# Kernel optimization log

Measured on AMD Instinct MI355X. Metric: run time of the kernel, lower is better.

Reference implementation:

```python
import jax, jax.numpy as jnp
import numpy as np
from jax import lax

B = 65536
N_STEPS = 256
WHEELBASE = 2.7
DT = 0.05
MAX_STEER = float(np.deg2rad(30.0))
MAX_SPEED = 100.0
FRICTION_ROAD = 0.1
FRICTION_AIR = 0.01


def setup_inputs() -> dict:
    key = jax.random.key(0)
    k1, k2, k3, k4, k5, k6 = jax.random.split(key, 6)
    return {
        "start_x": jax.random.normal(k1, (B,), dtype=jnp.float32),
        "start_y": jax.random.normal(k2, (B,), dtype=jnp.float32),
        "start_yaw": jax.random.normal(k3, (B,), dtype=jnp.float32),
        "start_speed": jax.random.uniform(k4, (B,), dtype=jnp.float32) * 20.0,
        "accel": jax.random.normal(k5, (B, N_STEPS), dtype=jnp.float32),
        "steering": jax.random.normal(k6, (B, N_STEPS), dtype=jnp.float32),
    }


def reference(start_x, start_y, start_yaw, start_speed, accel, steering):
    # One scan step = one iteration of the original python loop, vectorized over B.
    def step(carry, ctrl):
        x, y, yaw, sp = carry
        a, st = ctrl
        friction = sp * FRICTION_ROAD + FRICTION_AIR * sp * sp
        sp_next = jnp.clip(sp + DT * (a - friction), 0.0, MAX_SPEED)
        steer = jnp.clip(st, -MAX_STEER, MAX_STEER)
        ang_vel = sp * jnp.tan(steer) / WHEELBASE
        x_next = x + sp * jnp.cos(yaw) * DT
        y_next = y + sp * jnp.sin(yaw) * DT
        yaw_next = yaw + ang_vel * DT
        new = (x_next, y_next, yaw_next, sp_next)
        return new, new

    # Controls for steps 0..n_steps-2 (last control unused, as in the original loop).
    ctrls = (accel[:, : N_STEPS - 1].T, steering[:, : N_STEPS - 1].T)  # [T-1, B]
    init = (start_x, start_y, start_yaw, start_speed)
    _, traj = lax.scan(step, init, ctrls)  # each leaf [T-1, B]

    def full(s0, rest):
        return jnp.concatenate([s0[None, :], rest], axis=0).T  # [B, T]

    x = full(start_x, traj[0])
    y = full(start_y, traj[1])
    yaw = full(start_yaw, traj[2])
    speed = full(start_speed, traj[3])
    return (x, y, yaw, speed)
```

## Files before the change

### kernel.cpp

```cpp
#include <hip/hip_runtime.h>

#define T 256
#define TC 16
#define SC 32
#define NSC (T / SC)
#define V 64
#define DT 0.05f
#define WHEELBASE 2.7f
#define MAX_STEER 0.5235987755982988f
#define MAX_SPEED 100.0f
#define FR 0.1f
#define FA 0.01f

__device__ __forceinline__ void lds_fence() {
    asm volatile("s_waitcnt lgkmcnt(0)" ::: "memory");
}

__global__ __launch_bounds__(V) void bicycle_kernel(
    const float* __restrict__ sx, const float* __restrict__ sy,
    const float* __restrict__ syaw, const float* __restrict__ ssp,
    const float* __restrict__ accel, const float* __restrict__ steering,
    float* __restrict__ out, int B)
{
    __shared__ float lds[2][4][V][TC + 1];

    const int tid = threadIdx.x;
    const int b   = blockIdx.x * V + tid;

    float x   = sx[b];
    float y   = sy[b];
    float yaw = syaw[b];
    float sp  = ssp[b];

    const float4* a4 = (const float4*)(accel    + (size_t)b * T);
    const float4* s4 = (const float4*)(steering + (size_t)b * T);

    const size_t plane   = (size_t)B * T;
    const size_t vehBase = (size_t)blockIdx.x * V;

    const int u = tid >> 4;
    const int j = tid & 15;

    float4 av[SC / 4], sv[SC / 4], avn[SC / 4], svn[SC / 4];
    #pragma unroll
    for (int i = 0; i < SC / 4; ++i) { av[i] = a4[i]; sv[i] = s4[i]; }

    for (int c = 0; c < NSC; ++c) {
        if (c + 1 < NSC) {
            #pragma unroll
            for (int i = 0; i < SC / 4; ++i) {
                avn[i] = a4[(c + 1) * (SC / 4) + i];
                svn[i] = s4[(c + 1) * (SC / 4) + i];
            }
        }

        float ac[SC], scn[SC];
        #pragma unroll
        for (int i = 0; i < SC / 4; ++i) {
            ac[4*i+0]  = av[i].x; ac[4*i+1]  = av[i].y; ac[4*i+2]  = av[i].z; ac[4*i+3]  = av[i].w;
            scn[4*i+0] = sv[i].x; scn[4*i+1] = sv[i].y; scn[4*i+2] = sv[i].z; scn[4*i+3] = sv[i].w;
        }

        #pragma unroll
        for (int h = 0; h < 2; ++h) {
            const int buf = h;

            #pragma unroll
            for (int jj = 0; jj < TC; ++jj) {
                const int t = h * TC + jj;
                lds[buf][0][tid][jj] = x;
                lds[buf][1][tid][jj] = y;
                lds[buf][2][tid][jj] = yaw;
                lds[buf][3][tid][jj] = sp;

                float fr    = fmaf(FA * sp, sp, sp * FR);
                float spn   = fmaf(DT, ac[t] - fr, sp);
                spn         = fminf(fmaxf(spn, 0.0f), MAX_SPEED);
                float steer = fminf(fmaxf(scn[t], -MAX_STEER), MAX_STEER);
                float angv  = sp * __tanf(steer) * (1.0f / WHEELBASE);
                float s_, c_;
                __sincosf(yaw, &s_, &c_);
                float spDT = sp * DT;
                x   = fmaf(spDT, c_, x);
                y   = fmaf(spDT, s_, y);
                yaw = fmaf(angv, DT, yaw);
                sp  = spn;
            }

            lds_fence();

            const int t0 = c * SC + h * TC;
            #pragma unroll
            for (int p = 0; p < 4; ++p) {
                float* op = out + (size_t)p * plane + vehBase * T + t0;
                #pragma unroll
                for (int i = 0; i < TC; ++i) {
                    const int vv = i * 4 + u;
                    __builtin_nontemporal_store(lds[buf][p][vv][j],
                                                &op[(size_t)vv * T + j]);
                }
            }
        }

        if (c + 1 < NSC) {
            #pragma unroll
            for (int i = 0; i < SC / 4; ++i) { av[i] = avn[i]; sv[i] = svn[i]; }
        }
    }
}

extern "C" void kernel_launch(void* const* d_in, const int* in_sizes, int n_in,
                              void* d_out, int out_size, void* d_ws, size_t ws_size,
                              hipStream_t stream) {
    const float* sx       = (const float*)d_in[0];
    const float* sy       = (const float*)d_in[1];
    const float* syaw     = (const float*)d_in[2];
    const float* ssp      = (const float*)d_in[3];
    const float* steering = (const float*)d_in[5];
    const float* accel    = (const float*)d_in[4];
    float* out = (float*)d_out;

    int B = in_sizes[0];
    dim3 block(V);
    dim3 grid(B / V);
    hipLaunchKernelGGL(bicycle_kernel, grid, block, 0, stream,
                       sx, sy, syaw, ssp, accel, steering, out, B);
}
```

Baseline: 413.3 us.

## Coalesce control loads via LDS transpose and widen output store chunks

Control inputs are now loaded cooperatively: each group of 8 lanes reads 128 contiguous bytes of one vehicle's row. The tile is staged through shared memory with a padded pitch, then each thread reads back its own vehicle's 32 steps. This replaces per-thread strided float4 loads that were poorly coalesced. The state staging buffer now covers a full 32-step chunk instead of two 16-step halves, so stores write 128-byte row segments, and it reuses the same LDS pool as the controls. Because everything runs in one wave per block, the LDS reuse relies on waitcnt fences alone.

```diff
diff --git a/kernel.cpp b/kernel.cpp
--- a/kernel.cpp
+++ b/kernel.cpp
@@ -1,7 +1,6 @@
 #include <hip/hip_runtime.h>
 
 #define T 256
-#define TC 16
 #define SC 32
 #define NSC (T / SC)
 #define V 64
@@ -11,6 +10,9 @@
 #define MAX_SPEED 100.0f
 #define FR 0.1f
 #define FA 0.01f
+
+#define CTL_ROW_F4 9
+#define ST_PITCH  33
 
 __device__ __forceinline__ void lds_fence() {
     asm volatile("s_waitcnt lgkmcnt(0)" ::: "memory");
@@ -22,7 +24,9 @@
     const float* __restrict__ accel, const float* __restrict__ steering,
     float* __restrict__ out, int B)
 {
-    __shared__ float lds[2][4][V][TC + 1];
+    __shared__ float pool[4 * V * ST_PITCH];
+    float4* ctlA = (float4*)pool;
+    float4* ctlS = ctlA + V * CTL_ROW_F4;
 
     const int tid = threadIdx.x;
     const int b   = blockIdx.x * V + tid;
@@ -32,79 +36,89 @@
     float yaw = syaw[b];
     float sp  = ssp[b];
 
-    const float4* a4 = (const float4*)(accel    + (size_t)b * T);
-    const float4* s4 = (const float4*)(steering + (size_t)b * T);
+    const float4* gA = (const float4*)accel;
+    const float4* gS = (const float4*)steering;
 
     const size_t plane   = (size_t)B * T;
     const size_t vehBase = (size_t)blockIdx.x * V;
 
-    const int u = tid >> 4;
-    const int j = tid & 15;
+    const int lrow = tid >> 3;
+    const int lcol = tid & 7;
 
-    float4 av[SC / 4], sv[SC / 4], avn[SC / 4], svn[SC / 4];
+    const int wu = tid >> 5;
+    const int wj = tid & 31;
+
+    float4 avn[SC / 4], svn[SC / 4];
     #pragma unroll
-    for (int i = 0; i < SC / 4; ++i) { av[i] = a4[i]; sv[i] = s4[i]; }
+    for (int i = 0; i < SC / 4; ++i) {
+        const size_t r = vehBase + i * 8 + lrow;
+        avn[i] = gA[r * (T / 4) + lcol];
+        svn[i] = gS[r * (T / 4) + lcol];
+    }
 
     for (int c = 0; c < NSC; ++c) {
-        if (c + 1 < NSC) {
-            #pragma unroll
-            for (int i = 0; i < SC / 4; ++i) {
-                avn[i] = a4[(c + 1) * (SC / 4) + i];
-                svn[i] = s4[(c + 1) * (SC / 4) + i];
-            }
+        #pragma unroll
+        for (int i = 0; i < SC / 4; ++i) {
+            const int r = i * 8 + lrow;
+            ctlA[r * CTL_ROW_F4 + lcol] = avn[i];
+            ctlS[r * CTL_ROW_F4 + lcol] = svn[i];
         }
+        lds_fence();
 
+        float4 af4[SC / 4], sf4[SC / 4];
+        #pragma unroll
+        for (int k = 0; k < SC / 4; ++k) {
+            af4[k] = ctlA[tid * CTL_ROW_F4 + k];
+            sf4[k] = ctlS[tid * CTL_ROW_F4 + k];
+        }
         float ac[SC], scn[SC];
         #pragma unroll
-        for (int i = 0; i < SC / 4; ++i) {
-            ac[4*i+0]  = av[i].x; ac[4*i+1]  = av[i].y; ac[4*i+2]  = av[i].z; ac[4*i+3]  = av[i].w;
-            scn[4*i+0] = sv[i].x; scn[4*i+1] = sv[i].y; scn[4*i+2] = sv[i].z; scn[4*i+3] = sv[i].w;
-        }
-
-        #pragma unroll
-        for (int h = 0; h < 2; ++h) {
-            const int buf = h;
-
-            #pragma unroll
-            for (int jj = 0; jj < TC; ++jj) {
-                const int t = h * TC + jj;
-                lds[buf][0][tid][jj] = x;
-                lds[buf][1][tid][jj] = y;
-                lds[buf][2][tid][jj] = yaw;
-                lds[buf][3][tid][jj] = sp;
-
-                float fr    = fmaf(FA * sp, sp, sp * FR);
-                float spn   = fmaf(DT, ac[t] - fr, sp);
-                spn         = fminf(fmaxf(spn, 0.0f), MAX_SPEED);
-                float steer = fminf(fmaxf(scn[t], -MAX_STEER), MAX_STEER);
-                float angv  = sp * __tanf(steer) * (1.0f / WHEELBASE);
-                float s_, c_;
-                __sincosf(yaw, &s_, &c_);
-                float spDT = sp * DT;
-                x   = fmaf(spDT, c_, x);
-                y   = fmaf(spDT, s_, y);
-                yaw = fmaf(angv, DT, yaw);
-                sp  = spn;
-            }
-
-            lds_fence();
-
-            const int t0 = c * SC + h * TC;
-            #pragma unroll
-            for (int p = 0; p < 4; ++p) {
-                float* op = out + (size_t)p * plane + vehBase * T + t0;
-                #pragma unroll
-                for (int i = 0; i < TC; ++i) {
-                    const int vv = i * 4 + u;
-                    __builtin_nontemporal_store(lds[buf][p][vv][j],
-                                                &op[(size_t)vv * T + j]);
-                }
-            }
+        for (int k = 0; k < SC / 4; ++k) {
+            ac[4*k+0]  = af4[k].x; ac[4*k+1]  = af4[k].y; ac[4*k+2]  = af4[k].z; ac[4*k+3]  = af4[k].w;
+            scn[4*k+0] = sf4[k].x; scn[4*k+1] = sf4[k].y; scn[4*k+2] = sf4[k].z; scn[4*k+3] = sf4[k].w;
         }
 
         if (c + 1 < NSC) {
             #pragma unroll
-            for (int i = 0; i < SC / 4; ++i) { av[i] = avn[i]; sv[i] = svn[i]; }
+            for (int i = 0; i < SC / 4; ++i) {
+                const size_t r = vehBase + i * 8 + lrow;
+                avn[i] = gA[r * (T / 4) + (c + 1) * (SC / 4) + lcol];
+                svn[i] = gS[r * (T / 4) + (c + 1) * (SC / 4) + lcol];
+            }
+        }
+
+        #pragma unroll
+        for (int t = 0; t < SC; ++t) {
+            pool[(0 * V + tid) * ST_PITCH + t] = x;
+            pool[(1 * V + tid) * ST_PITCH + t] = y;
+            pool[(2 * V + tid) * ST_PITCH + t] = yaw;
+            pool[(3 * V + tid) * ST_PITCH + t] = sp;
+
+            float fr    = fmaf(FA * sp, sp, sp * FR);
+            float spn   = fmaf(DT, ac[t] - fr, sp);
+            spn         = fminf(fmaxf(spn, 0.0f), MAX_SPEED);
+            float steer = fminf(fmaxf(scn[t], -MAX_STEER), MAX_STEER);
+            float angv  = sp * __tanf(steer) * (1.0f / WHEELBASE);
+            float s_, c_;
+            __sincosf(yaw, &s_, &c_);
+            float spDT = sp * DT;
+            x   = fmaf(spDT, c_, x);
+            y   = fmaf(spDT, s_, y);
+            yaw = fmaf(angv, DT, yaw);
+            sp  = spn;
+        }
+        lds_fence();
+
+        const int t0 = c * SC;
+        #pragma unroll
+        for (int p = 0; p < 4; ++p) {
+            float* op = out + (size_t)p * plane + vehBase * T + t0;
+            #pragma unroll
+            for (int i = 0; i < V / 2; ++i) {
+                const int vv = i * 2 + wu;
+                __builtin_nontemporal_store(pool[(p * V + vv) * ST_PITCH + wj],
+                                            &op[(size_t)vv * T + wj]);
+            }
         }
     }
 }
@@ -116,8 +130,8 @@
     const float* sy       = (const float*)d_in[1];
     const float* syaw     = (const float*)d_in[2];
     const float* ssp      = (const float*)d_in[3];
+    const float* accel    = (const float*)d_in[4];
     const float* steering = (const float*)d_in[5];
-    const float* accel    = (const float*)d_in[4];
     float* out = (float*)d_out;
 
     int B = in_sizes[0];
```

Measured after the change: 511.2 us. 1.24x slower.
